# Performance work log

Measured on AMD Instinct MI355X. Metric: run time of the kernel, lower is better.

Reference implementation:

```python
import jax, jax.numpy as jnp
import numpy as np

EPS = 1e-8
SIM_THRESHOLD = 0.5


def _conv(x, src, dst, W, b):
    # Gather per-edge endpoint features: x_j = source, x_i = target (PyG default flow)
    x_j = x[src]
    x_i = x[dst]
    # Cosine similarity per edge
    dot = jnp.sum(x_i * x_j, axis=1)
    denom = jnp.maximum(jnp.linalg.norm(x_i, axis=1) * jnp.linalg.norm(x_j, axis=1), EPS)
    sim = dot / denom
    mask = (sim > SIM_THRESHOLD).astype(x.dtype)[:, None]
    msg = x_j * mask
    # Scatter-add aggregate into target nodes
    agg = jax.ops.segment_sum(msg, dst, num_segments=x.shape[0])
    # update: Linear
    return agg @ W.T + b


def setup_inputs() -> dict:
    key = jax.random.key(0)
    k1, k2, k3, k4, k5 = jax.random.split(key, 5)
    N, E, D_IN, D_HID, D_OUT = 50000, 800000, 128, 256, 64
    x = jax.random.normal(k1, (N, D_IN), dtype=jnp.float32)
    edge_index = jax.random.randint(k2, (2, E), 0, N, dtype=jnp.int64)
    # Xavier-uniform linear weights, zero-ish bias
    lim1 = float(np.sqrt(6.0 / (D_IN + D_HID)))
    lim2 = float(np.sqrt(6.0 / (D_HID + D_OUT)))
    W1 = jax.random.uniform(k3, (D_HID, D_IN), minval=-lim1, maxval=lim1, dtype=jnp.float32)
    b1 = jnp.zeros((D_HID,), dtype=jnp.float32)
    W2 = jax.random.uniform(k4, (D_OUT, D_HID), minval=-lim2, maxval=lim2, dtype=jnp.float32)
    b2 = jnp.zeros((D_OUT,), dtype=jnp.float32)
    return {"x": x, "edge_index": edge_index, "W1": W1, "b1": b1, "W2": W2, "b2": b2}


def reference(x, edge_index, W1, b1, W2, b2):
    N = x.shape[0]
    # add self-loops
    loops = jnp.arange(N, dtype=edge_index.dtype)
    src = jnp.concatenate([edge_index[0], loops])
    dst = jnp.concatenate([edge_index[1], loops])
    h = _conv(x, src, dst, W1, b1)
    h = jax.nn.relu(h)  # dropout is identity in eval mode
    out = _conv(h, src, dst, W2, b2)
    return jax.nn.log_softmax(out, axis=-1)
```

## Files before the change

kernel.cpp:

```cpp
#include <hip/hip_runtime.h>
#include <math.h>

#define EPS 1e-8f
#define NB_SORT 256

#if defined(__has_builtin)
#if __has_builtin(__builtin_amdgcn_sdot4)
#define HAVE_SDOT4 1
#endif
#endif

typedef __attribute__((ext_vector_type(8))) short bf16x8;
typedef __attribute__((ext_vector_type(4))) float f32x4;

__device__ __forceinline__ int sdot4i(int a, int b, int c) {
#ifdef HAVE_SDOT4
  return __builtin_amdgcn_sdot4(a, b, c, false);
#else
  return c + ((int)(signed char)(a)) * ((int)(signed char)(b)) +
         ((int)(signed char)(a >> 8)) * ((int)(signed char)(b >> 8)) +
         ((int)(signed char)(a >> 16)) * ((int)(signed char)(b >> 16)) +
         (a >> 24) * (b >> 24);
#endif
}

__device__ __forceinline__ float wave_reduce_sum(float v) {
#pragma unroll
  for (int off = 32; off > 0; off >>= 1)
    v += __shfl_xor(v, off, 64);
  return v;
}

__device__ __forceinline__ float wave_reduce_max(float v) {
#pragma unroll
  for (int off = 32; off > 0; off >>= 1)
    v = fmaxf(v, __shfl_xor(v, off, 64));
  return v;
}

__device__ __forceinline__ float dot4(float4 a, float4 b) {
  return a.x * b.x + a.y * b.y + a.z * b.z + a.w * b.w;
}

__device__ __forceinline__ int clampq(float q) {
  int i = (int)rintf(q);
  return i < -127 ? -127 : (i > 127 ? 127 : i);
}

__device__ __forceinline__ void split_bf16(float x, unsigned int& hi,
                                           unsigned int& lo) {
  unsigned int u = __float_as_uint(x);
  hi = u >> 16;
  float hf = __uint_as_float(u & 0xFFFF0000u);
  float r = x - hf;
  lo = __float_as_uint(r) >> 16;
}

__global__ __launch_bounds__(256) void hist_coarse(const int* __restrict__ dst,
                                                   int* __restrict__ hist_blk,
                                                   int E, int nbuck) {
  __shared__ int lh[1024];
  int t = threadIdx.x, blk = blockIdx.x;
  for (int i = t; i < nbuck; i += 256) lh[i] = 0;
  __syncthreads();
  int ch = (E + NB_SORT - 1) / NB_SORT;
  int lo = blk * ch, hi = min(E, lo + ch);
  for (int e = lo + t; e < hi; e += 256) atomicAdd(&lh[dst[e] >> 6], 1);
  __syncthreads();
  for (int i = t; i < nbuck; i += 256) hist_blk[i * NB_SORT + blk] = lh[i];
}

__global__ __launch_bounds__(256) void scan_local(int* __restrict__ hist,
                                                  int* __restrict__ bsum,
                                                  int nb) {
  __shared__ int tsum[256];
  int t = threadIdx.x;
  int base = blockIdx.x * 1024 + t * 4;
  int v0 = 0, v1 = 0, v2 = 0, v3 = 0;
  if (base + 3 < nb) {
    int4 q = *(const int4*)&hist[base];
    v0 = q.x; v1 = q.y; v2 = q.z; v3 = q.w;
  } else {
    if (base + 0 < nb) v0 = hist[base + 0];
    if (base + 1 < nb) v1 = hist[base + 1];
    if (base + 2 < nb) v2 = hist[base + 2];
  }
  tsum[t] = v0 + v1 + v2 + v3;
  __syncthreads();
  for (int off = 1; off < 256; off <<= 1) {
    int u = 0;
    if (t >= off) u = tsum[t - off];
    __syncthreads();
    if (t >= off) tsum[t] += u;
    __syncthreads();
  }
  int excl = (t == 0) ? 0 : tsum[t - 1];
  int e0 = excl, e1 = excl + v0, e2 = e1 + v1, e3 = e2 + v2;
  if (base + 3 < nb) {
    *(int4*)&hist[base] = make_int4(e0, e1, e2, e3);
  } else {
    if (base + 0 < nb) hist[base + 0] = e0;
    if (base + 1 < nb) hist[base + 1] = e1;
    if (base + 2 < nb) hist[base + 2] = e2;
  }
  if (t == 255) bsum[blockIdx.x] = tsum[255];
}

__global__ __launch_bounds__(256) void scan_bsum(int* __restrict__ bsum,
                                                 int nblk) {
  __shared__ int sh[256];
  int t = threadIdx.x;
  sh[t] = (t < nblk) ? bsum[t] : 0;
  __syncthreads();
  for (int off = 1; off < 256; off <<= 1) {
    int u = 0;
    if (t >= off) u = sh[t - off];
    __syncthreads();
    if (t >= off) sh[t] += u;
    __syncthreads();
  }
  if (t < nblk) bsum[t] = (t == 0) ? 0 : sh[t - 1];
}

__global__ __launch_bounds__(256) void add_bsum(int* __restrict__ hist,
                                                const int* __restrict__ bsum,
                                                int nb) {
  int i = blockIdx.x * blockDim.x + threadIdx.x;
  if (i < nb) hist[i] += bsum[i >> 10];
}

__global__ __launch_bounds__(256) void scatter_coarse(
    const int* __restrict__ src, const int* __restrict__ dst,
    const int* __restrict__ S, int2* __restrict__ epair, int E, int nbuck) {
  __shared__ int lb[1024];
  int t = threadIdx.x, blk = blockIdx.x;
  for (int i = t; i < nbuck; i += 256) lb[i] = S[i * NB_SORT + blk];
  __syncthreads();
  int ch = (E + NB_SORT - 1) / NB_SORT;
  int lo = blk * ch, hi = min(E, lo + ch);
  for (int e = lo + t; e < hi; e += 256) {
    int d = dst[e];
    int pos = atomicAdd(&lb[d >> 6], 1);
    epair[pos] = make_int2(src[e], d);
  }
}

__global__ __launch_bounds__(256) void fine_sort(
    const int2* __restrict__ epair, const int* __restrict__ S,
    int* __restrict__ ssrc, int* __restrict__ endoff, int E, int nbuck,
    int N) {
  __shared__ int fh[64];
  __shared__ int cur[64];
  int b = blockIdx.x, t = threadIdx.x;
  int bstart = S[b * NB_SORT];
  int bend = (b + 1 < nbuck) ? S[(b + 1) * NB_SORT] : E;
  if (t < 64) fh[t] = 0;
  __syncthreads();
  for (int e = bstart + t; e < bend; e += 256)
    atomicAdd(&fh[epair[e].y & 63], 1);
  __syncthreads();
  if (t < 64) {
    int v = fh[t];
    int incl = v;
#pragma unroll
    for (int off = 1; off < 64; off <<= 1) {
      int u = __shfl_up(incl, off, 64);
      if (t >= off) incl += u;
    }
    cur[t] = incl - v;
    int d = b * 64 + t;
    if (d < N) endoff[d] = bstart + incl;
  }
  __syncthreads();
  for (int e = bstart + t; e < bend; e += 256) {
    int2 p = epair[e];
    int pos = atomicAdd(&cur[p.y & 63], 1);
    ssrc[bstart + pos] = p.x;
  }
}

__global__ __launch_bounds__(256) void prep_x(const float* __restrict__ x,
                                              signed char* __restrict__ qx,
                                              float4* __restrict__ nprop,
                                              float* __restrict__ agg,
                                              int N) {
  int node = (int)((blockIdx.x * blockDim.x + threadIdx.x) >> 6);
  int lane = threadIdx.x & 63;
  if (node >= N) return;
  float2 v = *(const float2*)(x + (size_t)node * 128 + lane * 2);
  float ax = fabsf(v.x), ay = fabsf(v.y);
  float mx = wave_reduce_max(fmaxf(ax, ay));
  float l1 = wave_reduce_sum(ax + ay);
  float ss = wave_reduce_sum(v.x * v.x + v.y * v.y);
  float s = mx * (1.0f / 127.0f);
  float inv = (mx > 0.f) ? 127.0f / mx : 0.f;
  int q0 = clampq(v.x * inv), q1 = clampq(v.y * inv);
  unsigned short w = (unsigned short)((q0 & 0xff) | ((q1 & 0xff) << 8));
  ((unsigned short*)(qx + (size_t)node * 128))[lane] = w;
  float l1q = s * wave_reduce_sum((float)(abs(q0) + abs(q1)));
  bool sp = ss > 0.5f * fmaxf(ss, EPS);
  *(float2*)(agg + (size_t)node * 128 + lane * 2) =
      sp ? v : make_float2(0.f, 0.f);
  if (lane == 0)
    nprop[node] = make_float4(sqrtf(ss), s, fmaxf(l1, l1q), 0.f);
}

__global__ __launch_bounds__(256) void prep_h(const float* __restrict__ h,
                                              signed char* __restrict__ qh,
                                              float4* __restrict__ nprop,
                                              float* __restrict__ agg,
                                              int N) {
  int node = (int)((blockIdx.x * blockDim.x + threadIdx.x) >> 6);
  int lane = threadIdx.x & 63;
  if (node >= N) return;
  float4 v = *(const float4*)(h + (size_t)node * 256 + lane * 4);
  float ax = fabsf(v.x), ay = fabsf(v.y), az = fabsf(v.z), aw = fabsf(v.w);
  float mx = wave_reduce_max(fmaxf(fmaxf(ax, ay), fmaxf(az, aw)));
  float l1 = wave_reduce_sum(ax + ay + az + aw);
  float ss = wave_reduce_sum(dot4(v, v));
  float s = mx * (1.0f / 127.0f);
  float inv = (mx > 0.f) ? 127.0f / mx : 0.f;
  int q0 = clampq(v.x * inv), q1 = clampq(v.y * inv);
  int q2 = clampq(v.z * inv), q3 = clampq(v.w * inv);
  int w = (q0 & 0xff) | ((q1 & 0xff) << 8) | ((q2 & 0xff) << 16) | (q3 << 24);
  ((int*)(qh + (size_t)node * 256))[lane] = w;
  float l1q = s * wave_reduce_sum((float)(abs(q0) + abs(q1) + abs(q2) + abs(q3)));
  bool sp = ss > 0.5f * fmaxf(ss, EPS);
  *(float4*)(agg + (size_t)node * 256 + lane * 4) =
      sp ? v : make_float4(0.f, 0.f, 0.f, 0.f);
  if (lane == 0)
    nprop[node] = make_float4(sqrtf(ss), s, fmaxf(l1, l1q), 0.f);
}

template <int D>
__global__ __launch_bounds__(512) void conv_lpe(
    const float* __restrict__ xf, const signed char* __restrict__ qt,
    const float4* __restrict__ nprop, const int* __restrict__ ssrc,
    const int* __restrict__ endoff, float* __restrict__ agg, int N) {
  constexpr int RB = D + 16;
  constexpr int NG = D / 16;
  constexpr int V = D / 64;
  __shared__ signed char qtile[64 * RB];
  __shared__ float4 npd[64];
  __shared__ int eoff[65];
  const int tid = threadIdx.x;
  const int lane = tid & 63;
  const int n0 = blockIdx.x * 64;

  if (tid < 65) {
    int idx = n0 - 1 + tid;
    eoff[tid] = (idx < 0) ? 0 : endoff[min(idx, N - 1)];
  }
  if (tid >= 64 && tid < 128) {
    int i = tid - 64;
    int n = n0 + i;
    npd[i] = (n < N) ? nprop[n] : make_float4(0.f, 0.f, 0.f, 0.f);
  }
  for (int j = tid; j < 64 * NG; j += 512) {
    int r = j / NG, c = j % NG;
    int n = n0 + r;
    int4 v = (n < N) ? *(const int4*)(qt + (size_t)n * D + c * 16)
                     : make_int4(0, 0, 0, 0);
    *(int4*)(qtile + r * RB + c * 16) = v;
  }
  __syncthreads();

  const int bstart = eoff[0];
  const int bend = eoff[64];

  for (int base = bstart; base < bend; base += 512) {
    int e0 = base + tid;
    bool valid = e0 < bend;
    int s = valid ? ssrc[e0] : 0;
    float4 nps = valid ? nprop[s] : make_float4(0.f, 0.f, 0.f, 0.f);
    int lo = 0, hi = 63;
#pragma unroll
    for (int it = 0; it < 6; ++it) {
      int mid = (lo + hi) >> 1;
      if (e0 >= eoff[mid + 1]) lo = mid + 1; else hi = mid;
    }
    const int dloc = lo;
    float4 npdl = npd[dloc];
    const signed char* srow = qt + (size_t)s * D;
    const signed char* drow = qtile + dloc * RB;
    int id = 0;
#pragma unroll
    for (int g = 0; g < NG; ++g) {
      int4 a = *(const int4*)(srow + g * 16);
      int4 bq = *(const int4*)(drow + g * 16);
      id = sdot4i(a.x, bq.x, id);
      id = sdot4i(a.y, bq.y, id);
      id = sdot4i(a.z, bq.z, id);
      id = sdot4i(a.w, bq.w, id);
    }
    float denom = fmaxf(nps.x * npdl.x, EPS);
    float thr = 0.5f * denom;
    float approx = (nps.y * npdl.y) * (float)id;
    float m = 0.5002f * (nps.y * npdl.z + npdl.y * nps.z) + 2e-6f * denom + 1e-7f;
    bool maybe = valid && (approx > thr - m);
    unsigned long long mask = __ballot(maybe);
    while (mask) {
      int ln = __ffsll((long long)mask) - 1;
      mask &= mask - 1;
      int es = __shfl(s, ln);
      int dl = __shfl(dloc, ln);
      float nsx = __shfl(nps.x, ln);
      int dn = n0 + dl;
      float sv[V], dvv[V];
      if constexpr (V == 2) {
        float2 a = *(const float2*)(xf + (size_t)es * D + lane * 2);
        float2 b = *(const float2*)(xf + (size_t)dn * D + lane * 2);
        sv[0] = a.x; sv[1] = a.y; dvv[0] = b.x; dvv[1] = b.y;
      } else {
        float4 a = *(const float4*)(xf + (size_t)es * D + lane * 4);
        float4 b = *(const float4*)(xf + (size_t)dn * D + lane * 4);
        sv[0] = a.x; sv[1] = a.y; sv[2] = a.z; sv[3] = a.w;
        dvv[0] = b.x; dvv[1] = b.y; dvv[2] = b.z; dvv[3] = b.w;
      }
      float dx = 0.f;
#pragma unroll
      for (int q = 0; q < V; ++q) dx += sv[q] * dvv[q];
      dx = wave_reduce_sum(dx);
      float ndx = npd[dl].x;
      if (dx > 0.5f * fmaxf(nsx * ndx, EPS)) {
        float* arow = agg + (size_t)dn * D + lane * V;
#pragma unroll
        for (int q = 0; q < V; ++q) atomicAdd(&arow[q], sv[q]);
      }
    }
  }
}

__global__ __launch_bounds__(256) void gemm1_mfma(
    const float* __restrict__ A, const float* __restrict__ W,
    const float* __restrict__ bias, float* __restrict__ C, int M) {
  constexpr int K = 128, NN = 256, BM = 128, BK = 32, PK = 40;
  __shared__ unsigned short Ah[BM * PK];
  __shared__ unsigned short Al[BM * PK];
  __shared__ unsigned short Wh[BM * PK];
  __shared__ unsigned short Wl[BM * PK];
  const int tid = threadIdx.x;
  const int m0 = blockIdx.x * BM;
  const int n0 = blockIdx.y * BM;
  const int lane = tid & 63;
  const int wv = tid >> 6;
  const int wr = wv >> 1, wc = wv & 1;
  const int lrow = lane & 15, kg = lane >> 4;
  f32x4 acc[4][4] = {};

  for (int k0 = 0; k0 < K; k0 += BK) {
#pragma unroll
    for (int i = 0; i < 4; ++i) {
      int f = tid + i * 256;
      int r = f >> 3, q = f & 7;
      int gm = m0 + r;
      float4 a = (gm < M) ? *(const float4*)&A[(size_t)gm * K + k0 + q * 4]
                          : make_float4(0.f, 0.f, 0.f, 0.f);
      float4 w = *(const float4*)&W[(size_t)(n0 + r) * K + k0 + q * 4];
      unsigned int h0, h1, h2, h3, l0, l1, l2, l3;
      split_bf16(a.x, h0, l0); split_bf16(a.y, h1, l1);
      split_bf16(a.z, h2, l2); split_bf16(a.w, h3, l3);
      *(uint2*)&Ah[r * PK + q * 4] =
          make_uint2(h0 | (h1 << 16), h2 | (h3 << 16));
      *(uint2*)&Al[r * PK + q * 4] =
          make_uint2(l0 | (l1 << 16), l2 | (l3 << 16));
      split_bf16(w.x, h0, l0); split_bf16(w.y, h1, l1);
      split_bf16(w.z, h2, l2); split_bf16(w.w, h3, l3);
      *(uint2*)&Wh[r * PK + q * 4] =
          make_uint2(h0 | (h1 << 16), h2 | (h3 << 16));
      *(uint2*)&Wl[r * PK + q * 4] =
          make_uint2(l0 | (l1 << 16), l2 | (l3 << 16));
    }
    __syncthreads();
    bf16x8 ah[4], al[4], bh[4], bl[4];
#pragma unroll
    for (int m = 0; m < 4; ++m) {
      int row = wr * 64 + m * 16 + lrow;
      ah[m] = *(const bf16x8*)&Ah[row * PK + kg * 8];
      al[m] = *(const bf16x8*)&Al[row * PK + kg * 8];
    }
#pragma unroll
    for (int n = 0; n < 4; ++n) {
      int row = wc * 64 + n * 16 + lrow;
      bh[n] = *(const bf16x8*)&Wh[row * PK + kg * 8];
      bl[n] = *(const bf16x8*)&Wl[row * PK + kg * 8];
    }
#pragma unroll
    for (int m = 0; m < 4; ++m)
#pragma unroll
      for (int n = 0; n < 4; ++n) {
        acc[m][n] = __builtin_amdgcn_mfma_f32_16x16x32_bf16(ah[m], bh[n],
                                                            acc[m][n], 0, 0, 0);
        acc[m][n] = __builtin_amdgcn_mfma_f32_16x16x32_bf16(ah[m], bl[n],
                                                            acc[m][n], 0, 0, 0);
        acc[m][n] = __builtin_amdgcn_mfma_f32_16x16x32_bf16(al[m], bh[n],
                                                            acc[m][n], 0, 0, 0);
      }
    __syncthreads();
  }

#pragma unroll
  for (int n = 0; n < 4; ++n) {
    int gc = n0 + wc * 64 + n * 16 + lrow;
    float bv = bias[gc];
#pragma unroll
    for (int m = 0; m < 4; ++m) {
      int gr0 = m0 + wr * 64 + m * 16 + kg * 4;
#pragma unroll
      for (int r = 0; r < 4; ++r) {
        int gm = gr0 + r;
        if (gm < M) {
          float v = acc[m][n][r] + bv;
          C[(size_t)gm * NN + gc] = fmaxf(v, 0.f);
        }
      }
    }
  }
}

__global__ __launch_bounds__(256) void gemm2_lsm(
    const float* __restrict__ A, const float* __restrict__ W,
    const float* __restrict__ bias, float* __restrict__ out, int M, int K) {
  constexpr int BM = 128, BN = 64, BK = 32, TM = 4;
  constexpr int NTX = BN / 8;
  constexpr int KQ = BK / 4;
  constexpr int L4A = BM * KQ / 256;
  constexpr int L4B = BN * KQ / 256;
  constexpr int PM = BM + 4;
  constexpr int PN = BN + 4;
  __shared__ float smem[BM * 65];
  float* As = smem;
  float* Bs = smem + BK * PM;
  const int tid = threadIdx.x;
  const int m0 = blockIdx.x * BM;
  const int tx = tid % NTX;
  const int ty = tid / NTX;
  const int ms = ty * TM;
  const int ns = tx * 4;
  float acc[TM][8] = {};
  for (int k0 = 0; k0 < K; k0 += BK) {
#pragma unroll
    for (int t = 0; t < L4A; ++t) {
      int f = tid + t * 256;
      int row = (f >> 2) % BM;
      int kq = (f & 3) + 4 * (f / (4 * BM));
      int gm = m0 + row;
      float4 a = (gm < M) ? *(const float4*)&A[(size_t)gm * K + k0 + kq * 4]
                          : make_float4(0.f, 0.f, 0.f, 0.f);
      As[(kq * 4 + 0) * PM + row] = a.x; As[(kq * 4 + 1) * PM + row] = a.y;
      As[(kq * 4 + 2) * PM + row] = a.z; As[(kq * 4 + 3) * PM + row] = a.w;
    }
#pragma unroll
    for (int t = 0; t < L4B; ++t) {
      int f = tid + t * 256;
      int row = (f >> 2) % BN;
      int kq = (f & 3) + 4 * (f / (4 * BN));
      float4 b = *(const float4*)&W[(size_t)row * K + k0 + kq * 4];
      Bs[(kq * 4 + 0) * PN + row] = b.x; Bs[(kq * 4 + 1) * PN + row] = b.y;
      Bs[(kq * 4 + 2) * PN + row] = b.z; Bs[(kq * 4 + 3) * PN + row] = b.w;
    }
    __syncthreads();
#pragma unroll
    for (int kk = 0; kk < BK; ++kk) {
      float4 a4 = *(const float4*)&As[kk * PM + ms];
      float av[4] = {a4.x, a4.y, a4.z, a4.w};
      float4 b0 = *(const float4*)&Bs[kk * PN + ns];
      float4 b1 = *(const float4*)&Bs[kk * PN + ns + 32];
      float bv[8] = {b0.x, b0.y, b0.z, b0.w, b1.x, b1.y, b1.z, b1.w};
#pragma unroll
      for (int i = 0; i < TM; ++i)
#pragma unroll
        for (int j = 0; j < 8; ++j) acc[i][j] += av[i] * bv[j];
    }
    __syncthreads();
  }
  float4 bb0 = *(const float4*)&bias[ns];
  float4 bb1 = *(const float4*)&bias[32 + ns];
  float bv[8] = {bb0.x, bb0.y, bb0.z, bb0.w, bb1.x, bb1.y, bb1.z, bb1.w};
#pragma unroll
  for (int i = 0; i < TM; ++i) {
    int row = ms + i;
#pragma unroll
    for (int grp = 0; grp < 2; ++grp)
#pragma unroll
      for (int j = 0; j < 4; ++j)
        smem[row * 65 + grp * 32 + ns + j] = acc[i][grp * 4 + j] + bv[grp * 4 + j];
  }
  __syncthreads();
  int w = tid >> 6, lane = tid & 63;
  for (int r = w; r < BM; r += 4) {
    int gm = m0 + r;
    if (gm >= M) continue;
    float v = smem[r * 65 + lane];
    float mx = wave_reduce_max(v);
    float e = expf(v - mx);
    float sm = wave_reduce_sum(e);
    out[(size_t)gm * 64 + lane] = v - mx - logf(sm);
  }
}

extern "C" void kernel_launch(void* const* d_in, const int* in_sizes, int n_in,
                              void* d_out, int out_size, void* d_ws,
                              size_t ws_size, hipStream_t stream) {
  const float* x  = (const float*)d_in[0];
  const int* eidx = (const int*)d_in[1];
  const float* W1 = (const float*)d_in[2];
  const float* b1 = (const float*)d_in[3];
  const float* W2 = (const float*)d_in[4];
  const float* b2 = (const float*)d_in[5];
  float* out = (float*)d_out;

  const int N = in_sizes[0] / 128;
  const int E = in_sizes[1] / 2;
  const int* src = eidx;
  const int* dst = eidx + E;

  const int nbuck = (N + 63) / 64;
  const int ntot = nbuck * NB_SORT;
  const int nblk2 = (ntot + 1023) / 1024;

  float* agg    = (float*)d_ws;
  float* h      = agg + (size_t)N * 256;
  float4* npx   = (float4*)(h + (size_t)N * 256);
  float4* nph   = npx + N;
  int* S        = (int*)(nph + N);
  int* bsum     = S + ntot;
  int* ssrc     = bsum + 256;
  int* endoff   = ssrc + E;
  signed char* qh = (signed char*)(endoff + N);
  int2* epair   = (int2*)h;
  signed char* qx = (signed char*)(h + (size_t)N * 64);

  hist_coarse<<<NB_SORT, 256, 0, stream>>>(dst, S, E, nbuck);
  scan_local<<<nblk2, 256, 0, stream>>>(S, bsum, ntot);
  scan_bsum<<<1, 256, 0, stream>>>(bsum, nblk2);
  add_bsum<<<(ntot + 255) / 256, 256, 0, stream>>>(S, bsum, ntot);
  scatter_coarse<<<NB_SORT, 256, 0, stream>>>(src, dst, S, epair, E, nbuck);
  fine_sort<<<nbuck, 256, 0, stream>>>(epair, S, ssrc, endoff, E, nbuck, N);

  prep_x<<<(N + 3) / 4, 256, 0, stream>>>(x, qx, npx, agg, N);
  conv_lpe<128><<<nbuck, 512, 0, stream>>>(x, qx, npx, ssrc, endoff, agg, N);
  gemm1_mfma<<<dim3((N + 127) / 128, 2), 256, 0, stream>>>(agg, W1, b1, h, N);

  prep_h<<<(N + 3) / 4, 256, 0, stream>>>(h, qh, nph, agg, N);
  conv_lpe<256><<<nbuck, 512, 0, stream>>>(h, qh, nph, ssrc, endoff, agg, N);
  gemm2_lsm<<<dim3((N + 127) / 128), 256, 0, stream>>>(agg, W2, b2, out, N,
                                                       256);
}
```

Before: 322.2 us.

## Move second GEMM to split-bf16 MFMA with register-level log-softmax

Replaces the scalar FP32 tiled GEMM2 with an MFMA kernel. It splits both operands into high and low bf16 parts and sums three bf16 products to keep near-FP32 accuracy. A small pre-kernel splits W2 into bf16 halves each call. Log-softmax is now computed straight from the accumulator registers with lane shuffles, replacing the shared-memory staging pass. The trade-off is an extra launch and three MFMAs per tile. A rows are also loaded without a bounds check in the last block, which relies on workspace memory after agg being readable.

Result: faster. 300.6 us (-6.7%).

```diff
diff --git a/kernel.cpp b/kernel.cpp
--- a/kernel.cpp
+++ b/kernel.cpp
@@ -418,85 +418,103 @@
   }
 }
 
-__global__ __launch_bounds__(256) void gemm2_lsm(
-    const float* __restrict__ A, const float* __restrict__ W,
-    const float* __restrict__ bias, float* __restrict__ out, int M, int K) {
-  constexpr int BM = 128, BN = 64, BK = 32, TM = 4;
-  constexpr int NTX = BN / 8;
-  constexpr int KQ = BK / 4;
-  constexpr int L4A = BM * KQ / 256;
-  constexpr int L4B = BN * KQ / 256;
-  constexpr int PM = BM + 4;
-  constexpr int PN = BN + 4;
-  __shared__ float smem[BM * 65];
-  float* As = smem;
-  float* Bs = smem + BK * PM;
+__global__ __launch_bounds__(256) void split_w2(
+    const float* __restrict__ W, unsigned short* __restrict__ Wh,
+    unsigned short* __restrict__ Wl, int total4) {
+  int i = blockIdx.x * 256 + threadIdx.x;
+  if (i >= total4) return;
+  float4 w = ((const float4*)W)[i];
+  unsigned int h0, h1, h2, h3, l0, l1, l2, l3;
+  split_bf16(w.x, h0, l0); split_bf16(w.y, h1, l1);
+  split_bf16(w.z, h2, l2); split_bf16(w.w, h3, l3);
+  ((uint2*)Wh)[i] = make_uint2(h0 | (h1 << 16), h2 | (h3 << 16));
+  ((uint2*)Wl)[i] = make_uint2(l0 | (l1 << 16), l2 | (l3 << 16));
+}
+
+__global__ __launch_bounds__(256) void gemm2_mfma_lsm(
+    const float* __restrict__ A, const unsigned short* __restrict__ Wh,
+    const unsigned short* __restrict__ Wl, const float* __restrict__ bias,
+    float* __restrict__ out, int M) {
+  constexpr int K = 256;
   const int tid = threadIdx.x;
-  const int m0 = blockIdx.x * BM;
-  const int tx = tid % NTX;
-  const int ty = tid / NTX;
-  const int ms = ty * TM;
-  const int ns = tx * 4;
-  float acc[TM][8] = {};
-  for (int k0 = 0; k0 < K; k0 += BK) {
-#pragma unroll
-    for (int t = 0; t < L4A; ++t) {
-      int f = tid + t * 256;
-      int row = (f >> 2) % BM;
-      int kq = (f & 3) + 4 * (f / (4 * BM));
-      int gm = m0 + row;
-      float4 a = (gm < M) ? *(const float4*)&A[(size_t)gm * K + k0 + kq * 4]
-                          : make_float4(0.f, 0.f, 0.f, 0.f);
-      As[(kq * 4 + 0) * PM + row] = a.x; As[(kq * 4 + 1) * PM + row] = a.y;
-      As[(kq * 4 + 2) * PM + row] = a.z; As[(kq * 4 + 3) * PM + row] = a.w;
-    }
-#pragma unroll
-    for (int t = 0; t < L4B; ++t) {
-      int f = tid + t * 256;
-      int row = (f >> 2) % BN;
-      int kq = (f & 3) + 4 * (f / (4 * BN));
-      float4 b = *(const float4*)&W[(size_t)row * K + k0 + kq * 4];
-      Bs[(kq * 4 + 0) * PN + row] = b.x; Bs[(kq * 4 + 1) * PN + row] = b.y;
-      Bs[(kq * 4 + 2) * PN + row] = b.z; Bs[(kq * 4 + 3) * PN + row] = b.w;
-    }
-    __syncthreads();
-#pragma unroll
-    for (int kk = 0; kk < BK; ++kk) {
-      float4 a4 = *(const float4*)&As[kk * PM + ms];
-      float av[4] = {a4.x, a4.y, a4.z, a4.w};
-      float4 b0 = *(const float4*)&Bs[kk * PN + ns];
-      float4 b1 = *(const float4*)&Bs[kk * PN + ns + 32];
-      float bv[8] = {b0.x, b0.y, b0.z, b0.w, b1.x, b1.y, b1.z, b1.w};
-#pragma unroll
-      for (int i = 0; i < TM; ++i)
-#pragma unroll
-        for (int j = 0; j < 8; ++j) acc[i][j] += av[i] * bv[j];
-    }
-    __syncthreads();
-  }
-  float4 bb0 = *(const float4*)&bias[ns];
-  float4 bb1 = *(const float4*)&bias[32 + ns];
-  float bv[8] = {bb0.x, bb0.y, bb0.z, bb0.w, bb1.x, bb1.y, bb1.z, bb1.w};
-#pragma unroll
-  for (int i = 0; i < TM; ++i) {
-    int row = ms + i;
-#pragma unroll
-    for (int grp = 0; grp < 2; ++grp)
-#pragma unroll
-      for (int j = 0; j < 4; ++j)
-        smem[row * 65 + grp * 32 + ns + j] = acc[i][grp * 4 + j] + bv[grp * 4 + j];
-  }
-  __syncthreads();
-  int w = tid >> 6, lane = tid & 63;
-  for (int r = w; r < BM; r += 4) {
-    int gm = m0 + r;
-    if (gm >= M) continue;
-    float v = smem[r * 65 + lane];
-    float mx = wave_reduce_max(v);
-    float e = expf(v - mx);
-    float sm = wave_reduce_sum(e);
-    out[(size_t)gm * 64 + lane] = v - mx - logf(sm);
-  }
+  const int lane = tid & 63;
+  const int wv = tid >> 6;
+  const int lrow = lane & 15, kg = lane >> 4;
+  const int r0 = blockIdx.x * 128 + wv * 32;
+  f32x4 acc[2][4] = {};
+
+  for (int k0 = 0; k0 < K; k0 += 32) {
+    bf16x8 ah[2], al[2];
+#pragma unroll
+    for (int m = 0; m < 2; ++m) {
+      int row = r0 + m * 16 + lrow;
+      const float* ap = A + (size_t)row * K + k0 + kg * 8;
+      float4 a0 = *(const float4*)ap;
+      float4 a1 = *(const float4*)(ap + 4);
+      unsigned int hh[8], ll[8];
+      split_bf16(a0.x, hh[0], ll[0]); split_bf16(a0.y, hh[1], ll[1]);
+      split_bf16(a0.z, hh[2], ll[2]); split_bf16(a0.w, hh[3], ll[3]);
+      split_bf16(a1.x, hh[4], ll[4]); split_bf16(a1.y, hh[5], ll[5]);
+      split_bf16(a1.z, hh[6], ll[6]); split_bf16(a1.w, hh[7], ll[7]);
+      bf16x8 th, tl;
+#pragma unroll
+      for (int j = 0; j < 8; ++j) {
+        th[j] = (short)hh[j];
+        tl[j] = (short)ll[j];
+      }
+      ah[m] = th;
+      al[m] = tl;
+    }
+    bf16x8 bh[4], bl[4];
+#pragma unroll
+    for (int n = 0; n < 4; ++n) {
+      int wrow = n * 16 + lrow;
+      bh[n] = *(const bf16x8*)&Wh[(size_t)wrow * K + k0 + kg * 8];
+      bl[n] = *(const bf16x8*)&Wl[(size_t)wrow * K + k0 + kg * 8];
+    }
+#pragma unroll
+    for (int m = 0; m < 2; ++m)
+#pragma unroll
+      for (int n = 0; n < 4; ++n) {
+        acc[m][n] = __builtin_amdgcn_mfma_f32_16x16x32_bf16(ah[m], bh[n],
+                                                            acc[m][n], 0, 0, 0);
+        acc[m][n] = __builtin_amdgcn_mfma_f32_16x16x32_bf16(ah[m], bl[n],
+                                                            acc[m][n], 0, 0, 0);
+        acc[m][n] = __builtin_amdgcn_mfma_f32_16x16x32_bf16(al[m], bh[n],
+                                                            acc[m][n], 0, 0, 0);
+      }
+  }
+
+  float bv[4];
+#pragma unroll
+  for (int n = 0; n < 4; ++n) bv[n] = bias[n * 16 + lrow];
+#pragma unroll
+  for (int m = 0; m < 2; ++m)
+#pragma unroll
+    for (int r = 0; r < 4; ++r) {
+      int row = r0 + m * 16 + kg * 4 + r;
+      float v[4];
+      float mx = -1e30f;
+#pragma unroll
+      for (int n = 0; n < 4; ++n) {
+        v[n] = acc[m][n][r] + bv[n];
+        mx = fmaxf(mx, v[n]);
+      }
+#pragma unroll
+      for (int off = 8; off > 0; off >>= 1)
+        mx = fmaxf(mx, __shfl_xor(mx, off, 64));
+      float s = 0.f;
+#pragma unroll
+      for (int n = 0; n < 4; ++n) s += expf(v[n] - mx);
+#pragma unroll
+      for (int off = 8; off > 0; off >>= 1) s += __shfl_xor(s, off, 64);
+      float lg = logf(s);
+      if (row < M) {
+#pragma unroll
+        for (int n = 0; n < 4; ++n)
+          out[(size_t)row * 64 + n * 16 + lrow] = v[n] - mx - lg;
+      }
+    }
 }
 
 extern "C" void kernel_launch(void* const* d_in, const int* in_sizes, int n_in,
@@ -528,8 +546,12 @@
   int* ssrc     = bsum + 256;
   int* endoff   = ssrc + E;
   signed char* qh = (signed char*)(endoff + N);
+  unsigned short* W2h = (unsigned short*)(qh + (size_t)N * 256);
+  unsigned short* W2l = W2h + 64 * 256;
   int2* epair   = (int2*)h;
   signed char* qx = (signed char*)(h + (size_t)N * 64);
+
+  split_w2<<<16, 256, 0, stream>>>(W2, W2h, W2l, 64 * 256 / 4);
 
   hist_coarse<<<NB_SORT, 256, 0, stream>>>(dst, S, E, nbuck);
   scan_local<<<nblk2, 256, 0, stream>>>(S, bsum, ntot);
@@ -544,6 +566,6 @@
 
   prep_h<<<(N + 3) / 4, 256, 0, stream>>>(h, qh, nph, agg, N);
   conv_lpe<256><<<nbuck, 512, 0, stream>>>(h, qh, nph, ssrc, endoff, agg, N);
-  gemm2_lsm<<<dim3((N + 127) / 128), 256, 0, stream>>>(agg, W2, b2, out, N,
-                                                       256);
-}
+  gemm2_mfma_lsm<<<dim3((N + 127) / 128), 256, 0, stream>>>(agg, W2h, W2l, b2,
+                                                            out, N);
+}
```
